# Kernel optimization log

Measured on AMD Instinct MI355X. Metric: run time of the kernel, lower is better.

Reference implementation:

```python
import jax, jax.numpy as jnp
import numpy as np

N, E, DIM, L, NPERM, B = 20000, 640000, 128, 4, 20000, 256
R = NPERM * L * L  # rows of perm matrices
EPS = 1e-5


def _mlp(x, w1, b1, g, beta, w2, b2):
    # Linear -> BatchNorm (training-mode batch stats) -> ReLU -> Linear
    h = x @ w1 + b1
    mu = h.mean(0)
    var = h.var(0)  # biased, matches torch BN normalization
    h = (h - mu) * jax.lax.rsqrt(var + EPS) * g + beta
    return jax.nn.relu(h) @ w2 + b2


def setup_inputs() -> dict:
    key = jax.random.key(0)
    ks = jax.random.split(key, 40)
    s = 0.05
    inp = {}
    inp["node_feat"] = jax.random.normal(ks[0], (N, DIM), jnp.float32)
    inp["edge_feat"] = jax.random.normal(ks[1], (E, DIM), jnp.float32)
    inp["src"] = jax.random.randint(ks[2], (E,), 0, N)
    inp["dst"] = jax.random.randint(ks[3], (E,), 0, N)
    inp["rev_flag"] = jax.random.randint(ks[4], (E,), 0, 2).astype(bool)
    # sparse node_to_perm / edge_to_perm: one nnz per row (row i implicit)
    inp["n2p_cols"] = jax.random.randint(ks[5], (R,), 0, N)
    inp["n2p_vals"] = jax.random.uniform(ks[6], (R,), jnp.float32)
    inp["e2p_cols"] = jax.random.randint(ks[7], (R,), 0, E)
    inp["e2p_vals"] = jax.random.uniform(ks[8], (R,), jnp.float32)
    # sparse pooling matrix: perm j -> graph pool_rows[j] with weight pool_vals[j]
    inp["pool_rows"] = jax.random.randint(ks[9], (NPERM,), 0, B)
    inp["pool_vals"] = jax.random.uniform(ks[10], (NPERM,), jnp.float32)
    for i, n in enumerate(["in_w", "out_w", "src_w", "dst_w", "nloop_w", "eloop_w"]):
        inp[n] = jax.random.normal(ks[11 + i], (DIM, DIM), jnp.float32) * s
    inp["lrp_w"] = jax.random.normal(ks[17], (DIM, DIM, L * L), jnp.float32) * s
    inp["nbias"] = jnp.zeros((DIM,), jnp.float32)
    inp["ebias"] = jnp.zeros((DIM,), jnp.float32)
    inp["lrp_bias"] = jnp.zeros((DIM,), jnp.float32)
    for p, k0 in (("n", 20), ("e", 26)):
        inp[p + "mlp_w1"] = jax.random.normal(ks[k0], (DIM, DIM), jnp.float32) * s
        inp[p + "mlp_b1"] = jnp.zeros((DIM,), jnp.float32)
        inp[p + "mlp_g"] = jnp.ones((DIM,), jnp.float32)
        inp[p + "mlp_beta"] = jnp.zeros((DIM,), jnp.float32)
        inp[p + "mlp_w2"] = jax.random.normal(ks[k0 + 1], (DIM, DIM), jnp.float32) * s
        inp[p + "mlp_b2"] = jnp.zeros((DIM,), jnp.float32)
    return inp


def reference(node_feat, edge_feat, src, dst, rev_flag, n2p_cols, n2p_vals,
              e2p_cols, e2p_vals, pool_rows, pool_vals,
              in_w, out_w, src_w, dst_w, nloop_w, eloop_w, lrp_w,
              nbias, ebias, lrp_bias,
              nmlp_w1, nmlp_b1, nmlp_g, nmlp_beta, nmlp_w2, nmlp_b2,
              emlp_w1, emlp_b1, emlp_g, emlp_beta, emlp_w2, emlp_b2):
    hs = node_feat[src]   # [E, d]
    hd = node_feat[dst]   # [E, d]
    r = rev_flag[:, None]
    # per-edge messages with reverse-edge masking
    edge_msg = jnp.where(r, hs @ dst_w - hd @ src_w, hd @ dst_w - hs @ src_w)
    node_msg = jnp.where(r, edge_feat @ out_w, -(edge_feat @ in_w))
    node_agg = jax.ops.segment_sum(node_msg, dst, num_segments=N)
    # node update
    nout = _mlp(node_feat @ nloop_w + node_agg + nbias,
                nmlp_w1, nmlp_b1, nmlp_g, nmlp_beta, nmlp_w2, nmlp_b2)
    # edge update: degree-scaled term uses out-degree of dst node
    out_deg = jax.ops.segment_sum(jnp.ones((E,), jnp.float32), src, num_segments=N)
    dlog = jnp.log2(1.0 + out_deg[dst])[:, None]
    add = 2.0 * (1.0 + dlog) * (edge_feat @ (src_w - dst_w))
    eout = _mlp(edge_feat @ eloop_w + add + edge_msg + ebias,
                emlp_w1, emlp_b1, emlp_g, emlp_beta, emlp_w2, emlp_b2)
    # sparse perm gathers + LRP einsum + sparse pooling scatter
    perm = n2p_vals[:, None] * nout[n2p_cols] + e2p_vals[:, None] * eout[e2p_cols]
    perm = perm.reshape(NPERM, L * L, DIM)
    lrp = jnp.einsum('dab,bca->dc', perm, lrp_w) + lrp_bias
    pooled = jax.ops.segment_sum(pool_vals[:, None] * lrp, pool_rows, num_segments=B)
    return pooled, eout
```

## Files before the change

### kernel.cpp

```cpp
#include <hip/hip_runtime.h>
#include <stdint.h>

constexpr int Nn     = 20000;
constexpr int Ee     = 640000;
constexpr int NPERMc = 20000;

using bf16x8 = __attribute__((ext_vector_type(8))) short;
using f32x4  = __attribute__((ext_vector_type(4))) float;
using s16x4  = __attribute__((ext_vector_type(4))) short;
using u16x8  = __attribute__((ext_vector_type(8))) unsigned short;

__device__ __forceinline__ short f2bf(float f) {
  union { float f; unsigned u; } v; v.f = f;
  unsigned r = v.u + 0x7FFFu + ((v.u >> 16) & 1u);
  return (short)(r >> 16);
}
__device__ __forceinline__ float bf2f(unsigned short s) {
  union { unsigned u; float f; } v; v.u = ((unsigned)s) << 16;
  return v.f;
}
__device__ __forceinline__ f32x4 MFMA(bf16x8 a, bf16x8 b, f32x4 c) {
  return __builtin_amdgcn_mfma_f32_16x16x32_bf16(a, b, c, 0, 0, 0);
}

__device__ __forceinline__ int swz(int s) { return s ^ (((s >> 7) & 7) << 3); }

__device__ __forceinline__ int fragIdx(int k, int n) {
  int t = n >> 4, kk = k >> 5;
  int l = ((k & 31) >> 3) * 16 + (n & 15);
  int j = k & 7;
  return ((t * 4 + kk) * 64 + l) * 8 + j;
}

__device__ __forceinline__ void stage16x128(const float* __restrict__ src, int row0, int M,
                                            int lane, short* lds) {
  #pragma unroll
  for (int it = 0; it < 8; ++it) {
    int u = it * 64 + lane;
    int r = u >> 5;
    int q = u & 31;
    int row = row0 + r;
    float4 v = make_float4(0.f, 0.f, 0.f, 0.f);
    if (row < M) v = ((const float4*)(src + (size_t)row * 128))[q];
    int k  = q * 4;
    int kk = k >> 5;
    int l2 = ((k & 31) >> 3) * 16 + r;
    int j  = k & 7;
    s16x4 s4 = { f2bf(v.x), f2bf(v.y), f2bf(v.z), f2bf(v.w) };
    *(s16x4*)(lds + swz((kk * 64 + l2) * 8 + j)) = s4;
  }
}

__global__ __launch_bounds__(256) void kPrep(
    const float* __restrict__ in_w,  const float* __restrict__ out_w,
    const float* __restrict__ src_w, const float* __restrict__ dst_w,
    const float* __restrict__ nloop_w, const float* __restrict__ eloop_w,
    const float* __restrict__ lrp_w,
    const float* __restrict__ nbias, const float* __restrict__ ebias,
    const float* __restrict__ w1e, const float* __restrict__ b1e,
    const float* __restrict__ w1n, const float* __restrict__ b1n,
    const float* __restrict__ w2e, const float* __restrict__ w2n,
    short* __restrict__ WA, short* __restrict__ BQ, short* __restrict__ WN,
    short* __restrict__ W2E, short* __restrict__ W2N, short* __restrict__ WL,
    float* __restrict__ c0e, float* __restrict__ c0n) {
  __shared__ float Rl[16384];
  int tid = threadIdx.x;
  int blk = blockIdx.x;
  if (blk < 448) {
    int p = blk >> 6, sub = blk & 63;
    const float* La; const float* Lb = nullptr; const float* R; short* outp;
    float sOut = 1.f;
    switch (p) {
      case 0: La = eloop_w;             R = w1e; outp = WA;          break;
      case 1: La = src_w; Lb = dst_w;   R = w1e; outp = WA + 16384;  break;
      case 2: La = dst_w;               R = w1e; outp = BQ;          break;
      case 3: La = src_w;               R = w1e; outp = BQ + 16384;  break;
      case 4: La = nloop_w;             R = w1n; outp = WN;          break;
      case 5: La = out_w;               R = w1n; outp = WN + 16384;  break;
      default: La = in_w;               R = w1n; outp = WN + 32768; sOut = -1.f; break;
    }
    for (int i = tid; i < 16384; i += 256) Rl[i] = R[i];
    __syncthreads();
    int e = sub * 256 + tid;
    int k = e >> 7, n = e & 127;
    float acc = 0.f;
    bool hasLb = (Lb != nullptr);
    for (int j = 0; j < 128; ++j) {
      float l = La[k * 128 + j];
      if (hasLb) l -= Lb[k * 128 + j];
      acc += l * Rl[j * 128 + n];
    }
    outp[fragIdx(k, n)] = f2bf(acc * sOut);
  } else if (blk < 512) {
    int e = (blk - 448) * 256 + tid; int k = e >> 7, n = e & 127;
    W2E[fragIdx(k, n)] = f2bf(w2e[k * 128 + n]);
  } else if (blk < 576) {
    int e = (blk - 512) * 256 + tid; int k = e >> 7, n = e & 127;
    W2N[fragIdx(k, n)] = f2bf(w2n[k * 128 + n]);
  } else if (blk < 1600) {
    int q = blk - 576; int a = q >> 6;
    int e = (q & 63) * 256 + tid; int k = e >> 7, n = e & 127;
    WL[a * 16384 + fragIdx(k, n)] = f2bf(lrp_w[(k * 128 + n) * 16 + a]);
  } else {
    if (tid < 128) {
      float acc = 0.f;
      for (int k2 = 0; k2 < 128; ++k2) acc += ebias[k2] * w1e[k2 * 128 + tid];
      c0e[tid] = acc + b1e[tid];
    } else {
      int n = tid - 128; float acc = 0.f;
      for (int k2 = 0; k2 < 128; ++k2) acc += nbias[k2] * w1n[k2 * 128 + n];
      c0n[n] = acc + b1n[n];
    }
  }
}


__global__ __launch_bounds__(256) void kHist(
    const int* __restrict__ srcI, const int* __restrict__ dstI,
    int* __restrict__ cnt, float* __restrict__ deg) {
  int e = blockIdx.x * 256 + threadIdx.x;
  atomicAdd(&cnt[dstI[e]], 1);
  atomicAdd(&deg[srcI[e]], 1.0f);
}

__global__ __launch_bounds__(256) void kScan(const int* __restrict__ cnt,
                                             int* __restrict__ off,
                                             int* __restrict__ cur) {
  __shared__ int lc[Nn];
  __shared__ int ps[256];
  int tid = threadIdx.x;
  for (int i = tid; i < Nn; i += 256) lc[i] = cnt[i];
  __syncthreads();
  constexpr int CH = (Nn + 255) / 256;
  int base = tid * CH;
  int local = 0;
  for (int i = 0; i < CH; ++i) {
    int idx = base + i;
    if (idx < Nn) local += lc[idx];
  }
  ps[tid] = local;
  __syncthreads();
  for (int d = 1; d < 256; d <<= 1) {
    int t = (tid >= d) ? ps[tid - d] : 0;
    __syncthreads();
    if (tid >= d) ps[tid] += t;
    __syncthreads();
  }
  int run = ps[tid] - local;
  for (int i = 0; i < CH; ++i) {
    int idx = base + i;
    if (idx < Nn) { off[idx] = run; cur[idx] = run; run += lc[idx]; }
  }
}

__global__ __launch_bounds__(256) void kScatter(
    const int* __restrict__ dstI, const int* __restrict__ revI,
    int* __restrict__ cur, int* __restrict__ order) {
  int e = blockIdx.x * 256 + threadIdx.x;
  int pos = atomicAdd(&cur[dstI[e]], 1);
  order[pos] = revI[e] ? (e | (int)0x80000000) : e;
}

__global__ __launch_bounds__(256) void kAgg2(
    const float* __restrict__ ef, const int* __restrict__ off,
    const int* __restrict__ cnt, const int* __restrict__ order,
    float* __restrict__ aggR, float* __restrict__ aggN) {
  int w = threadIdx.x >> 6, lane = threadIdx.x & 63;
  int n = blockIdx.x * 4 + w;
  if (n >= Nn) return;
  int s0 = off[n], c = cnt[n];
  float2 aR = make_float2(0.f, 0.f), aN = make_float2(0.f, 0.f);
  int i = 0;
  for (; i + 1 < c; i += 2) {
    int oe0 = order[s0 + i];
    int oe1 = order[s0 + i + 1];
    int e0 = oe0 & 0x7fffffff;
    int e1 = oe1 & 0x7fffffff;
    float2 v0 = ((const float2*)(ef + (size_t)e0 * 128))[lane];
    float2 v1 = ((const float2*)(ef + (size_t)e1 * 128))[lane];
    if (oe0 < 0) { aR.x += v0.x; aR.y += v0.y; } else { aN.x += v0.x; aN.y += v0.y; }
    if (oe1 < 0) { aR.x += v1.x; aR.y += v1.y; } else { aN.x += v1.x; aN.y += v1.y; }
  }
  if (i < c) {
    int oe = order[s0 + i];
    int e = oe & 0x7fffffff;
    float2 v = ((const float2*)(ef + (size_t)e * 128))[lane];
    if (oe < 0) { aR.x += v.x; aR.y += v.y; } else { aN.x += v.x; aN.y += v.y; }
  }
  ((float2*)(aggR + (size_t)n * 128))[lane] = aR;
  ((float2*)(aggN + (size_t)n * 128))[lane] = aN;
}

__global__ __launch_bounds__(256, 2) void kQ(const float* __restrict__ nf,
                                             const short* __restrict__ BQ,
                                             float* __restrict__ Q, int M) {
  __shared__ __align__(16) short alds[4][2048];
  __shared__ __align__(16) short wbuf[8192];
  int tid = threadIdx.x, w = tid >> 6, lane = tid & 63;
  int row0 = blockIdx.x * 64 + w * 16;
  stage16x128(nf, row0, M, lane, alds[w]);
  f32x4 acc[16];
  #pragma unroll
  for (int t = 0; t < 16; ++t) acc[t] = (f32x4){0.f, 0.f, 0.f, 0.f};
  const int4* g4 = (const int4*)BQ;
  for (int kk = 0; kk < 4; ++kk) {
    __syncthreads();
    for (int c = tid; c < 1024; c += 256) {
      int t = c >> 6, l = c & 63;
      ((int4*)wbuf)[c] = g4[(t * 4 + kk) * 64 + l];
    }
    __syncthreads();
    bf16x8 a = *(const bf16x8*)(alds[w] + swz((kk * 64 + lane) * 8));
    #pragma unroll
    for (int t = 0; t < 16; ++t) {
      bf16x8 b = *(const bf16x8*)(wbuf + (t * 64 + lane) * 8);
      acc[t] = MFMA(a, b, acc[t]);
    }
  }
  int sub = lane >> 4, m = lane & 15;
  #pragma unroll
  for (int i = 0; i < 4; ++i) {
    int row = row0 + sub * 4 + i;
    if (row < M) {
      #pragma unroll
      for (int h = 0; h < 2; ++h) {
        float4 f0, f1;
        f0.x = acc[h * 8 + 0][i]; f0.y = acc[h * 8 + 1][i];
        f0.z = acc[h * 8 + 2][i]; f0.w = acc[h * 8 + 3][i];
        f1.x = acc[h * 8 + 4][i]; f1.y = acc[h * 8 + 5][i];
        f1.z = acc[h * 8 + 6][i]; f1.w = acc[h * 8 + 7][i];
        float4* dst = (float4*)(Q + (size_t)row * 256 + h * 128 + m * 8);
        dst[0] = f0; dst[1] = f1;
      }
    }
  }
}

__global__ __launch_bounds__(256, 2) void kN1(
    const float* __restrict__ nf, const float* __restrict__ aggR,
    const float* __restrict__ aggN, const short* __restrict__ WN,
    const float* __restrict__ c0n, short* __restrict__ hN,
    float* __restrict__ scratchN, int M) {
  __shared__ __align__(16) short alds[4][2048];
  __shared__ __align__(16) short wlds[16384];
  __shared__ float statsLDS[256];
  int tid = threadIdx.x, w = tid >> 6, lane = tid & 63;
  int m = lane & 15, sub = lane >> 4;
  statsLDS[tid] = 0.f;
  int row0 = blockIdx.x * 64 + w * 16;
  f32x4 acc[8];
  #pragma unroll
  for (int t = 0; t < 8; ++t) acc[t] = (f32x4){0.f, 0.f, 0.f, 0.f};
  for (int s = 0; s < 3; ++s) {
    const float* src = (s == 0) ? nf : ((s == 1) ? aggR : aggN);
    __syncthreads();
    const int4* g4 = (const int4*)(WN + s * 16384);
    for (int c = tid; c < 2048; c += 256) ((int4*)wlds)[c] = g4[c];
    __syncthreads();
    stage16x128(src, row0, M, lane, alds[w]);
    for (int kk = 0; kk < 4; ++kk) {
      bf16x8 a = *(const bf16x8*)(alds[w] + swz((kk * 64 + lane) * 8));
      #pragma unroll
      for (int t = 0; t < 8; ++t) {
        bf16x8 b = *(const bf16x8*)(wlds + ((t * 4 + kk) * 64 + lane) * 8);
        acc[t] = MFMA(a, b, acc[t]);
      }
    }
  }
  float c0v[8];
  #pragma unroll
  for (int t = 0; t < 8; ++t) c0v[t] = c0n[t * 16 + m];
  float ss[8], sq[8];
  #pragma unroll
  for (int t = 0; t < 8; ++t) { ss[t] = 0.f; sq[t] = 0.f; }
  #pragma unroll
  for (int i = 0; i < 4; ++i) {
    int row = row0 + sub * 4 + i;
    if (row < M) {
      bf16x8 pk;
      #pragma unroll
      for (int t = 0; t < 8; ++t) {
        float h = acc[t][i] + c0v[t];
        pk[t] = f2bf(h); ss[t] += h; sq[t] += h * h;
      }
      *(bf16x8*)(hN + (size_t)row * 128 + m * 8) = pk;
    }
  }
  #pragma unroll
  for (int t = 0; t < 8; ++t) {
    float a = ss[t], b = sq[t];
    a += __shfl_xor(a, 16, 64); b += __shfl_xor(b, 16, 64);
    a += __shfl_xor(a, 32, 64); b += __shfl_xor(b, 32, 64);
    if (lane < 16) {
      atomicAdd(&statsLDS[t * 16 + lane], a);
      atomicAdd(&statsLDS[128 + t * 16 + lane], b);
    }
  }
  __syncthreads();
  scratchN[(size_t)tid * gridDim.x + blockIdx.x] = statsLDS[tid];
}

__global__ __launch_bounds__(256, 2) void kD(
    const float* __restrict__ ef, const short* __restrict__ WA,
    const float* __restrict__ Q, const float* __restrict__ c0e,
    const int* __restrict__ srcI, const int* __restrict__ dstI,
    const int* __restrict__ revI, const float* __restrict__ deg,
    short* __restrict__ hE, float* __restrict__ scratchE) {
  __shared__ __align__(16) short alds[4][4096];
  __shared__ __align__(16) short wbuf[8192];
  __shared__ float statsLDS[256];
  int tid = threadIdx.x, w = tid >> 6, lane = tid & 63;
  int m = lane & 15, sub = lane >> 4;
  statsLDS[tid] = 0.f;
  int row0 = blockIdx.x * 128 + w * 32;
  float scl[8]; int qa[8], qb[8];
  #pragma unroll
  for (int g = 0; g < 2; ++g)
    #pragma unroll
    for (int i = 0; i < 4; ++i) {
      int e = row0 + g * 16 + sub * 4 + i;
      int s_ = srcI[e], d_ = dstI[e], r_ = revI[e];
      int x = g * 4 + i;
      scl[x] = 2.0f * (1.0f + log2f(1.0f + deg[d_]));
      int na = r_ ? s_ : d_;
      int nb = r_ ? d_ : s_;
      qa[x] = na * 256 + m * 8;
      qb[x] = nb * 256 + 128 + m * 8;
    }
  stage16x128(ef, row0,      Ee, lane, alds[w]);
  stage16x128(ef, row0 + 16, Ee, lane, alds[w] + 2048);
  f32x4 acc1[2][8], acc2[2][8];
  #pragma unroll
  for (int g = 0; g < 2; ++g)
    #pragma unroll
    for (int t = 0; t < 8; ++t) { acc1[g][t] = (f32x4){0,0,0,0}; acc2[g][t] = (f32x4){0,0,0,0}; }
  const int4* g4 = (const int4*)WA;
  for (int kk = 0; kk < 4; ++kk) {
    __syncthreads();
    for (int c = tid; c < 1024; c += 256) {
      int mm = c >> 9, t = (c >> 6) & 7, l = c & 63;
      ((int4*)wbuf)[c] = g4[mm * 2048 + (t * 4 + kk) * 64 + l];
    }
    __syncthreads();
    bf16x8 a0 = *(const bf16x8*)(alds[w] + swz((kk * 64 + lane) * 8));
    bf16x8 a1 = *(const bf16x8*)(alds[w] + 2048 + swz((kk * 64 + lane) * 8));
    #pragma unroll
    for (int t = 0; t < 8; ++t) {
      bf16x8 b1 = *(const bf16x8*)(wbuf + (t * 64 + lane) * 8);
      bf16x8 b2 = *(const bf16x8*)(wbuf + 4096 + (t * 64 + lane) * 8);
      acc1[0][t] = MFMA(a0, b1, acc1[0][t]);
      acc1[1][t] = MFMA(a1, b1, acc1[1][t]);
      acc2[0][t] = MFMA(a0, b2, acc2[0][t]);
      acc2[1][t] = MFMA(a1, b2, acc2[1][t]);
    }
  }
  float c0v[8];
  #pragma unroll
  for (int t = 0; t < 8; ++t) c0v[t] = c0e[t * 16 + m];
  float ss[8], sq[8];
  #pragma unroll
  for (int t = 0; t < 8; ++t) { ss[t] = 0.f; sq[t] = 0.f; }
  #pragma unroll
  for (int g = 0; g < 2; ++g) {
    #pragma unroll
    for (int i = 0; i < 4; ++i) {
      int x = g * 4 + i;
      int e = row0 + g * 16 + sub * 4 + i;
      float4 A0 = ((const float4*)(Q + qa[x]))[0];
      float4 A1 = ((const float4*)(Q + qa[x]))[1];
      float4 B0 = ((const float4*)(Q + qb[x]))[0];
      float4 B1 = ((const float4*)(Q + qb[x]))[1];
      float qv[8] = {A0.x - B0.x, A0.y - B0.y, A0.z - B0.z, A0.w - B0.w,
                     A1.x - B1.x, A1.y - B1.y, A1.z - B1.z, A1.w - B1.w};
      bf16x8 pk;
      #pragma unroll
      for (int t = 0; t < 8; ++t) {
        float h = acc1[g][t][i] + scl[x] * acc2[g][t][i] + qv[t] + c0v[t];
        pk[t] = f2bf(h);
        ss[t] += h; sq[t] += h * h;
      }
      *(bf16x8*)(hE + (size_t)e * 128 + m * 8) = pk;
    }
  }
  #pragma unroll
  for (int t = 0; t < 8; ++t) {
    float a = ss[t], b = sq[t];
    a += __shfl_xor(a, 16, 64); b += __shfl_xor(b, 16, 64);
    a += __shfl_xor(a, 32, 64); b += __shfl_xor(b, 32, 64);
    if (lane < 16) {
      atomicAdd(&statsLDS[t * 16 + lane], a);
      atomicAdd(&statsLDS[128 + t * 16 + lane], b);
    }
  }
  __syncthreads();
  scratchE[(size_t)tid * gridDim.x + blockIdx.x] = statsLDS[tid];
}

__global__ __launch_bounds__(256) void kFin(const float* __restrict__ scratch, int NB,
                                            float M, const float* __restrict__ g,
                                            const float* __restrict__ beta,
                                            float* __restrict__ st) {
  __shared__ float red[256];
  __shared__ float red2[256];
  int c = blockIdx.x;
  int tid = threadIdx.x;
  float s = 0.f, q = 0.f;
  for (int i = tid; i < NB; i += 256) {
    s += scratch[(size_t)c * NB + i];
    q += scratch[(size_t)(128 + c) * NB + i];
  }
  red[tid] = s; red2[tid] = q;
  __syncthreads();
  for (int off = 128; off > 0; off >>= 1) {
    if (tid < off) { red[tid] += red[tid + off]; red2[tid] += red2[tid + off]; }
    __syncthreads();
  }
  if (tid == 0) {
    float mu  = red[0] / M;
    float var = red2[0] / M - mu * mu;
    float inv = rsqrtf(var + 1e-5f);
    float sc  = g[c] * inv;
    st[c] = sc;
    st[128 + c] = beta[c] - mu * sc;
  }
}

__global__ __launch_bounds__(256, 2) void kF(const short* __restrict__ h,
                                             const float* __restrict__ st,
                                             const short* __restrict__ w2f,
                                             const float* __restrict__ b2,
                                             float* __restrict__ outp, int M) {
  __shared__ __align__(16) short alds[4][2048];
  __shared__ __align__(16) short wlds[16384];
  int tid = threadIdx.x, w = tid >> 6, lane = tid & 63;
  int m2 = lane & 15;
  for (int c = tid; c < 2048; c += 256) ((int4*)wlds)[c] = ((const int4*)w2f)[c];
  int row0 = blockIdx.x * 64 + w * 16;
  float sc8[8], tb8[8];
  #pragma unroll
  for (int q = 0; q < 8; ++q) {
    int col = q * 16 + m2;
    sc8[q] = st[col]; tb8[q] = st[128 + col];
  }
  #pragma unroll
  for (int it = 0; it < 4; ++it) {
    int r = it * 4 + (lane >> 4);
    int row = row0 + r;
    u16x8 hv = {0, 0, 0, 0, 0, 0, 0, 0};
    if (row < M) hv = *(const u16x8*)(h + (size_t)row * 128 + m2 * 8);
    #pragma unroll
    for (int q = 0; q < 8; ++q) {
      float f = bf2f(hv[q]);
      float v = fmaxf(f * sc8[q] + tb8[q], 0.f);
      int k = q * 16 + m2;
      int kk = k >> 5, l2 = ((k & 31) >> 3) * 16 + r, j = k & 7;
      alds[w][swz((kk * 64 + l2) * 8 + j)] = f2bf(v);
    }
  }
  __syncthreads();
  f32x4 acc[8];
  #pragma unroll
  for (int t = 0; t < 8; ++t) acc[t] = (f32x4){0.f, 0.f, 0.f, 0.f};
  for (int kk = 0; kk < 4; ++kk) {
    bf16x8 a = *(const bf16x8*)(alds[w] + swz((kk * 64 + lane) * 8));
    #pragma unroll
    for (int t = 0; t < 8; ++t) {
      bf16x8 b = *(const bf16x8*)(wlds + ((t * 4 + kk) * 64 + lane) * 8);
      acc[t] = MFMA(a, b, acc[t]);
    }
  }
  int sub = lane >> 4;
  #pragma unroll
  for (int t = 0; t < 8; ++t) {
    int col = t * 16 + (lane & 15);
    float bb = b2[col];
    #pragma unroll
    for (int i = 0; i < 4; ++i) {
      int row = row0 + sub * 4 + i;
      if (row < M) outp[(size_t)row * 128 + col] = acc[t][i] + bb;
    }
  }
}

__global__ __launch_bounds__(256, 2) void kLRP(
    const float* __restrict__ nout, const float* __restrict__ eoutp,
    const int* __restrict__ n2pc, const float* __restrict__ n2pv,
    const int* __restrict__ e2pc, const float* __restrict__ e2pv,
    const int* __restrict__ poolr, const float* __restrict__ poolv,
    const short* __restrict__ WL, const float* __restrict__ lrp_bias,
    float* __restrict__ pooled) {
  __shared__ __align__(16) short alds[4][2048];
  __shared__ __align__(16) short wlds[16384];
  int tid = threadIdx.x, w = tid >> 6, lane = tid & 63;
  int row0 = blockIdx.x * 64 + w * 16;
  f32x4 acc[8];
  #pragma unroll
  for (int t = 0; t < 8; ++t) acc[t] = (f32x4){0.f, 0.f, 0.f, 0.f};
  for (int a = 0; a < 16; ++a) {
    __syncthreads();
    const int4* g4 = (const int4*)(WL + a * 16384);
    for (int c = tid; c < 2048; c += 256) ((int4*)wlds)[c] = g4[c];
    __syncthreads();
    #pragma unroll
    for (int it = 0; it < 8; ++it) {
      int u = it * 64 + lane;
      int r = u >> 5;
      int q = u & 31;
      int d = row0 + r;
      float4 v = make_float4(0.f, 0.f, 0.f, 0.f);
      if (d < NPERMc) {
        int i = d * 16 + a;
        int nc = n2pc[i]; float nv = n2pv[i];
        int ec = e2pc[i]; float ev = e2pv[i];
        float4 nr = ((const float4*)(nout  + (size_t)nc * 128))[q];
        float4 er = ((const float4*)(eoutp + (size_t)ec * 128))[q];
        v.x = nv * nr.x + ev * er.x;
        v.y = nv * nr.y + ev * er.y;
        v.z = nv * nr.z + ev * er.z;
        v.w = nv * nr.w + ev * er.w;
      }
      int k  = q * 4;
      int kk = k >> 5;
      int l2 = ((k & 31) >> 3) * 16 + r;
      int j  = k & 7;
      s16x4 s4 = { f2bf(v.x), f2bf(v.y), f2bf(v.z), f2bf(v.w) };
      *(s16x4*)(alds[w] + swz((kk * 64 + l2) * 8 + j)) = s4;
    }
    for (int kk = 0; kk < 4; ++kk) {
      bf16x8 aa = *(const bf16x8*)(alds[w] + swz((kk * 64 + lane) * 8));
      #pragma unroll
      for (int t = 0; t < 8; ++t) {
        bf16x8 b = *(const bf16x8*)(wlds + ((t * 4 + kk) * 64 + lane) * 8);
        acc[t] = MFMA(aa, b, acc[t]);
      }
    }
  }
  int sub = lane >> 4;
  #pragma unroll
  for (int t = 0; t < 8; ++t) {
    int col = t * 16 + (lane & 15);
    float lb = lrp_bias[col];
    #pragma unroll
    for (int i = 0; i < 4; ++i) {
      int d = row0 + sub * 4 + i;
      if (d < NPERMc) {
        float val = acc[t][i] + lb;
        atomicAdd(&pooled[poolr[d] * 128 + col], poolv[d] * val);
      }
    }
  }
}

extern "C" void kernel_launch(void* const* d_in, const int* in_sizes, int n_in,
                              void* d_out, int out_size, void* d_ws, size_t ws_size,
                              hipStream_t stream) {
  (void)in_sizes; (void)n_in; (void)out_size; (void)ws_size;
  const float* node_feat = (const float*)d_in[0];
  const float* edge_feat = (const float*)d_in[1];
  const int*   srcI      = (const int*)d_in[2];
  const int*   dstI      = (const int*)d_in[3];
  const int*   revI      = (const int*)d_in[4];
  const int*   n2pc      = (const int*)d_in[5];
  const float* n2pv      = (const float*)d_in[6];
  const int*   e2pc      = (const int*)d_in[7];
  const float* e2pv      = (const float*)d_in[8];
  const int*   poolr     = (const int*)d_in[9];
  const float* poolv     = (const float*)d_in[10];
  const float* in_w      = (const float*)d_in[11];
  const float* out_w     = (const float*)d_in[12];
  const float* src_w     = (const float*)d_in[13];
  const float* dst_w     = (const float*)d_in[14];
  const float* nloop_w   = (const float*)d_in[15];
  const float* eloop_w   = (const float*)d_in[16];
  const float* lrp_w     = (const float*)d_in[17];
  const float* nbias     = (const float*)d_in[18];
  const float* ebias     = (const float*)d_in[19];
  const float* lrp_bias  = (const float*)d_in[20];
  const float* nmlp_w1   = (const float*)d_in[21];
  const float* nmlp_b1   = (const float*)d_in[22];
  const float* nmlp_g    = (const float*)d_in[23];
  const float* nmlp_beta = (const float*)d_in[24];
  const float* nmlp_w2   = (const float*)d_in[25];
  const float* nmlp_b2   = (const float*)d_in[26];
  const float* emlp_w1   = (const float*)d_in[27];
  const float* emlp_b1   = (const float*)d_in[28];
  const float* emlp_g    = (const float*)d_in[29];
  const float* emlp_beta = (const float*)d_in[30];
  const float* emlp_w2   = (const float*)d_in[31];
  const float* emlp_b2   = (const float*)d_in[32];

  float* pooled = (float*)d_out;
  float* eoutp  = (float*)d_out + 32768;

  char* p = (char*)d_ws;
  auto alloc = [&](size_t b) { char* r = p; p += (b + 255) & ~(size_t)255; return r; };
  short* hE   = (short*)alloc((size_t)Ee * 128 * 2);
  float* Qm   = (float*)alloc((size_t)Nn * 256 * 4);
  float* aggR = (float*)alloc((size_t)Nn * 128 * 4);
  float* aggN = (float*)alloc((size_t)Nn * 128 * 4);
  short* hN   = (short*)alloc((size_t)Nn * 128 * 2);
  float* nout = (float*)alloc((size_t)Nn * 128 * 4);
  float* deg  = (float*)alloc((size_t)Nn * 4);
  float* scrE = (float*)alloc((size_t)256 * 5000 * 4);
  float* scrN = (float*)alloc((size_t)256 * 313 * 4);
  float* stE  = (float*)alloc(256 * 4);
  float* stN  = (float*)alloc(256 * 4);
  short* WA   = (short*)alloc(32768 * 2);
  short* BQ   = (short*)alloc(32768 * 2);
  short* WN   = (short*)alloc(49152 * 2);
  short* W2E  = (short*)alloc(16384 * 2);
  short* W2N  = (short*)alloc(16384 * 2);
  short* WL   = (short*)alloc((size_t)16 * 16384 * 2);
  float* c0e  = (float*)alloc(128 * 4);
  float* c0n  = (float*)alloc(128 * 4);
  int*   cnt  = (int*)alloc((size_t)Nn * 4);
  int*   offA = (int*)alloc((size_t)Nn * 4);
  int*   cur  = (int*)alloc((size_t)Nn * 4);
  int*   order= (int*)alloc((size_t)Ee * 4);

  hipMemsetAsync(deg,  0, (size_t)Nn * 4, stream);
  hipMemsetAsync(cnt,  0, (size_t)Nn * 4, stream);
  hipMemsetAsync(pooled, 0, (size_t)32768 * 4, stream);

  kPrep<<<1601, 256, 0, stream>>>(in_w, out_w, src_w, dst_w, nloop_w, eloop_w, lrp_w,
                                  nbias, ebias, emlp_w1, emlp_b1, nmlp_w1, nmlp_b1,
                                  emlp_w2, nmlp_w2, WA, BQ, WN, W2E, W2N, WL, c0e, c0n);
  kHist<<<Ee / 256, 256, 0, stream>>>(srcI, dstI, cnt, deg);
  kScan<<<1, 256, 0, stream>>>(cnt, offA, cur);
  kScatter<<<Ee / 256, 256, 0, stream>>>(dstI, revI, cur, order);
  kAgg2<<<Nn / 4, 256, 0, stream>>>(edge_feat, offA, cnt, order, aggR, aggN);
  kQ<<<313, 256, 0, stream>>>(node_feat, BQ, Qm, Nn);
  kN1<<<313, 256, 0, stream>>>(node_feat, aggR, aggN, WN, c0n, hN, scrN, Nn);
  kD<<<5000, 256, 0, stream>>>(edge_feat, WA, Qm, c0e, srcI, dstI, revI, deg, hE, scrE);
  kFin<<<128, 256, 0, stream>>>(scrE, 5000, (float)Ee, emlp_g, emlp_beta, stE);
  kFin<<<128, 256, 0, stream>>>(scrN, 313, (float)Nn, nmlp_g, nmlp_beta, stN);
  kF<<<10000, 256, 0, stream>>>(hE, stE, W2E, emlp_b2, eoutp, Ee);
  kF<<<313, 256, 0, stream>>>(hN, stN, W2N, nmlp_b2, nout, Nn);
  kLRP<<<313, 256, 0, stream>>>(nout, eoutp, n2pc, n2pv, e2pc, e2pv,
                                poolr, poolv, WL, lrp_bias, pooled);
}
```

Before: 1.419 ms.

## Shrink kD tiles for occupancy, split kLRP over a-groups, unroll kAgg2 by four

kD now processes 16 rows per wave instead of 32, which halves its LDS and accumulator footprint, doubles the grid and raises launch bounds to 4 blocks per CU. The cost is that each weight chunk is reused across fewer rows. kLRP is split into 4 groups over the a dimension, giving 4x more blocks and relying on the existing pooled atomics to combine partial sums. kAgg2 unrolls its gather loop to 4 edges for more loads in flight. The trade-off is more weight staging traffic and more atomic contention on pooled.

```diff
diff --git a/kernel.cpp b/kernel.cpp
--- a/kernel.cpp
+++ b/kernel.cpp
@@ -171,17 +171,21 @@
   int s0 = off[n], c = cnt[n];
   float2 aR = make_float2(0.f, 0.f), aN = make_float2(0.f, 0.f);
   int i = 0;
-  for (; i + 1 < c; i += 2) {
+  for (; i + 3 < c; i += 4) {
     int oe0 = order[s0 + i];
     int oe1 = order[s0 + i + 1];
-    int e0 = oe0 & 0x7fffffff;
-    int e1 = oe1 & 0x7fffffff;
-    float2 v0 = ((const float2*)(ef + (size_t)e0 * 128))[lane];
-    float2 v1 = ((const float2*)(ef + (size_t)e1 * 128))[lane];
+    int oe2 = order[s0 + i + 2];
+    int oe3 = order[s0 + i + 3];
+    float2 v0 = ((const float2*)(ef + (size_t)(oe0 & 0x7fffffff) * 128))[lane];
+    float2 v1 = ((const float2*)(ef + (size_t)(oe1 & 0x7fffffff) * 128))[lane];
+    float2 v2 = ((const float2*)(ef + (size_t)(oe2 & 0x7fffffff) * 128))[lane];
+    float2 v3 = ((const float2*)(ef + (size_t)(oe3 & 0x7fffffff) * 128))[lane];
     if (oe0 < 0) { aR.x += v0.x; aR.y += v0.y; } else { aN.x += v0.x; aN.y += v0.y; }
     if (oe1 < 0) { aR.x += v1.x; aR.y += v1.y; } else { aN.x += v1.x; aN.y += v1.y; }
-  }
-  if (i < c) {
+    if (oe2 < 0) { aR.x += v2.x; aR.y += v2.y; } else { aN.x += v2.x; aN.y += v2.y; }
+    if (oe3 < 0) { aR.x += v3.x; aR.y += v3.y; } else { aN.x += v3.x; aN.y += v3.y; }
+  }
+  for (; i < c; ++i) {
     int oe = order[s0 + i];
     int e = oe & 0x7fffffff;
     float2 v = ((const float2*)(ef + (size_t)e * 128))[lane];
@@ -300,40 +304,34 @@
   scratchN[(size_t)tid * gridDim.x + blockIdx.x] = statsLDS[tid];
 }
 
-__global__ __launch_bounds__(256, 2) void kD(
+__global__ __launch_bounds__(256, 4) void kD(
     const float* __restrict__ ef, const short* __restrict__ WA,
     const float* __restrict__ Q, const float* __restrict__ c0e,
     const int* __restrict__ srcI, const int* __restrict__ dstI,
     const int* __restrict__ revI, const float* __restrict__ deg,
     short* __restrict__ hE, float* __restrict__ scratchE) {
-  __shared__ __align__(16) short alds[4][4096];
+  __shared__ __align__(16) short alds[4][2048];
   __shared__ __align__(16) short wbuf[8192];
   __shared__ float statsLDS[256];
   int tid = threadIdx.x, w = tid >> 6, lane = tid & 63;
   int m = lane & 15, sub = lane >> 4;
   statsLDS[tid] = 0.f;
-  int row0 = blockIdx.x * 128 + w * 32;
-  float scl[8]; int qa[8], qb[8];
-  #pragma unroll
-  for (int g = 0; g < 2; ++g)
-    #pragma unroll
-    for (int i = 0; i < 4; ++i) {
-      int e = row0 + g * 16 + sub * 4 + i;
-      int s_ = srcI[e], d_ = dstI[e], r_ = revI[e];
-      int x = g * 4 + i;
-      scl[x] = 2.0f * (1.0f + log2f(1.0f + deg[d_]));
-      int na = r_ ? s_ : d_;
-      int nb = r_ ? d_ : s_;
-      qa[x] = na * 256 + m * 8;
-      qb[x] = nb * 256 + 128 + m * 8;
-    }
-  stage16x128(ef, row0,      Ee, lane, alds[w]);
-  stage16x128(ef, row0 + 16, Ee, lane, alds[w] + 2048);
-  f32x4 acc1[2][8], acc2[2][8];
-  #pragma unroll
-  for (int g = 0; g < 2; ++g)
-    #pragma unroll
-    for (int t = 0; t < 8; ++t) { acc1[g][t] = (f32x4){0,0,0,0}; acc2[g][t] = (f32x4){0,0,0,0}; }
+  int row0 = blockIdx.x * 64 + w * 16;
+  float scl[4]; int qa[4], qb[4];
+  #pragma unroll
+  for (int i = 0; i < 4; ++i) {
+    int e = row0 + sub * 4 + i;
+    int s_ = srcI[e], d_ = dstI[e], r_ = revI[e];
+    scl[i] = 2.0f * (1.0f + log2f(1.0f + deg[d_]));
+    int na = r_ ? s_ : d_;
+    int nb = r_ ? d_ : s_;
+    qa[i] = na * 256 + m * 8;
+    qb[i] = nb * 256 + 128 + m * 8;
+  }
+  stage16x128(ef, row0, Ee, lane, alds[w]);
+  f32x4 acc1[8], acc2[8];
+  #pragma unroll
+  for (int t = 0; t < 8; ++t) { acc1[t] = (f32x4){0,0,0,0}; acc2[t] = (f32x4){0,0,0,0}; }
   const int4* g4 = (const int4*)WA;
   for (int kk = 0; kk < 4; ++kk) {
     __syncthreads();
@@ -342,16 +340,13 @@
       ((int4*)wbuf)[c] = g4[mm * 2048 + (t * 4 + kk) * 64 + l];
     }
     __syncthreads();
-    bf16x8 a0 = *(const bf16x8*)(alds[w] + swz((kk * 64 + lane) * 8));
-    bf16x8 a1 = *(const bf16x8*)(alds[w] + 2048 + swz((kk * 64 + lane) * 8));
+    bf16x8 a = *(const bf16x8*)(alds[w] + swz((kk * 64 + lane) * 8));
     #pragma unroll
     for (int t = 0; t < 8; ++t) {
       bf16x8 b1 = *(const bf16x8*)(wbuf + (t * 64 + lane) * 8);
       bf16x8 b2 = *(const bf16x8*)(wbuf + 4096 + (t * 64 + lane) * 8);
-      acc1[0][t] = MFMA(a0, b1, acc1[0][t]);
-      acc1[1][t] = MFMA(a1, b1, acc1[1][t]);
-      acc2[0][t] = MFMA(a0, b2, acc2[0][t]);
-      acc2[1][t] = MFMA(a1, b2, acc2[1][t]);
+      acc1[t] = MFMA(a, b1, acc1[t]);
+      acc2[t] = MFMA(a, b2, acc2[t]);
     }
   }
   float c0v[8];
@@ -361,26 +356,22 @@
   #pragma unroll
   for (int t = 0; t < 8; ++t) { ss[t] = 0.f; sq[t] = 0.f; }
   #pragma unroll
-  for (int g = 0; g < 2; ++g) {
-    #pragma unroll
-    for (int i = 0; i < 4; ++i) {
-      int x = g * 4 + i;
-      int e = row0 + g * 16 + sub * 4 + i;
-      float4 A0 = ((const float4*)(Q + qa[x]))[0];
-      float4 A1 = ((const float4*)(Q + qa[x]))[1];
-      float4 B0 = ((const float4*)(Q + qb[x]))[0];
-      float4 B1 = ((const float4*)(Q + qb[x]))[1];
-      float qv[8] = {A0.x - B0.x, A0.y - B0.y, A0.z - B0.z, A0.w - B0.w,
-                     A1.x - B1.x, A1.y - B1.y, A1.z - B1.z, A1.w - B1.w};
-      bf16x8 pk;
-      #pragma unroll
-      for (int t = 0; t < 8; ++t) {
-        float h = acc1[g][t][i] + scl[x] * acc2[g][t][i] + qv[t] + c0v[t];
-        pk[t] = f2bf(h);
-        ss[t] += h; sq[t] += h * h;
-      }
-      *(bf16x8*)(hE + (size_t)e * 128 + m * 8) = pk;
-    }
+  for (int i = 0; i < 4; ++i) {
+    int e = row0 + sub * 4 + i;
+    float4 A0 = ((const float4*)(Q + qa[i]))[0];
+    float4 A1 = ((const float4*)(Q + qa[i]))[1];
+    float4 B0 = ((const float4*)(Q + qb[i]))[0];
+    float4 B1 = ((const float4*)(Q + qb[i]))[1];
+    float qv[8] = {A0.x - B0.x, A0.y - B0.y, A0.z - B0.z, A0.w - B0.w,
+                   A1.x - B1.x, A1.y - B1.y, A1.z - B1.z, A1.w - B1.w};
+    bf16x8 pk;
+    #pragma unroll
+    for (int t = 0; t < 8; ++t) {
+      float h = acc1[t][i] + scl[i] * acc2[t][i] + qv[t] + c0v[t];
+      pk[t] = f2bf(h);
+      ss[t] += h; sq[t] += h * h;
+    }
+    *(bf16x8*)(hE + (size_t)e * 128 + m * 8) = pk;
   }
   #pragma unroll
   for (int t = 0; t < 8; ++t) {
@@ -492,11 +483,13 @@
   __shared__ __align__(16) short alds[4][2048];
   __shared__ __align__(16) short wlds[16384];
   int tid = threadIdx.x, w = tid >> 6, lane = tid & 63;
-  int row0 = blockIdx.x * 64 + w * 16;
+  int blk = blockIdx.x % 313, g = blockIdx.x / 313;
+  int row0 = blk * 64 + w * 16;
+  int a0 = g * 4;
   f32x4 acc[8];
   #pragma unroll
   for (int t = 0; t < 8; ++t) acc[t] = (f32x4){0.f, 0.f, 0.f, 0.f};
-  for (int a = 0; a < 16; ++a) {
+  for (int a = a0; a < a0 + 4; ++a) {
     __syncthreads();
     const int4* g4 = (const int4*)(WL + a * 16384);
     for (int c = tid; c < 2048; c += 256) ((int4*)wlds)[c] = g4[c];
@@ -539,7 +532,7 @@
   #pragma unroll
   for (int t = 0; t < 8; ++t) {
     int col = t * 16 + (lane & 15);
-    float lb = lrp_bias[col];
+    float lb = (g == 0) ? lrp_bias[col] : 0.f;
     #pragma unroll
     for (int i = 0; i < 4; ++i) {
       int d = row0 + sub * 4 + i;
@@ -601,7 +594,7 @@
   short* hN   = (short*)alloc((size_t)Nn * 128 * 2);
   float* nout = (float*)alloc((size_t)Nn * 128 * 4);
   float* deg  = (float*)alloc((size_t)Nn * 4);
-  float* scrE = (float*)alloc((size_t)256 * 5000 * 4);
+  float* scrE = (float*)alloc((size_t)256 * 10000 * 4);
   float* scrN = (float*)alloc((size_t)256 * 313 * 4);
   float* stE  = (float*)alloc(256 * 4);
   float* stN  = (float*)alloc(256 * 4);
@@ -631,11 +624,11 @@
   kAgg2<<<Nn / 4, 256, 0, stream>>>(edge_feat, offA, cnt, order, aggR, aggN);
   kQ<<<313, 256, 0, stream>>>(node_feat, BQ, Qm, Nn);
   kN1<<<313, 256, 0, stream>>>(node_feat, aggR, aggN, WN, c0n, hN, scrN, Nn);
-  kD<<<5000, 256, 0, stream>>>(edge_feat, WA, Qm, c0e, srcI, dstI, revI, deg, hE, scrE);
-  kFin<<<128, 256, 0, stream>>>(scrE, 5000, (float)Ee, emlp_g, emlp_beta, stE);
+  kD<<<10000, 256, 0, stream>>>(edge_feat, WA, Qm, c0e, srcI, dstI, revI, deg, hE, scrE);
+  kFin<<<128, 256, 0, stream>>>(scrE, 10000, (float)Ee, emlp_g, emlp_beta, stE);
   kFin<<<128, 256, 0, stream>>>(scrN, 313, (float)Nn, nmlp_g, nmlp_beta, stN);
   kF<<<10000, 256, 0, stream>>>(hE, stE, W2E, emlp_b2, eoutp, Ee);
   kF<<<313, 256, 0, stream>>>(hN, stN, W2N, nmlp_b2, nout, Nn);
-  kLRP<<<313, 256, 0, stream>>>(nout, eoutp, n2pc, n2pv, e2pc, e2pv,
-                                poolr, poolv, WL, lrp_bias, pooled);
-}
+  kLRP<<<1252, 256, 0, stream>>>(nout, eoutp, n2pc, n2pv, e2pc, e2pv,
+                                 poolr, poolv, WL, lrp_bias, pooled);
+}
```

Measured after the change: 1.358 ms. -4.2%, faster.
